# Optimization experiments

Measured on AMD Instinct MI355X. Metric: run time of the kernel, lower is better.

The kernel has to match this reference:

```python
import jax, jax.numpy as jnp
import numpy as np

NEG_SLOPE = 0.01
EPS = 1e-5


def leaky_relu(x):
    return jnp.where(x >= 0, x, NEG_SLOPE * x)


def graph_conv(x, W, src, dst, edge_weight, num_nodes):
    # DGL GraphConv, norm='both', bias=False: D_out^{-1/2} A_w D_in^{-1/2} X W
    ones = jnp.ones_like(edge_weight)
    deg_out = jnp.maximum(jax.ops.segment_sum(ones, src, num_segments=num_nodes), 1.0)
    deg_in = jnp.maximum(jax.ops.segment_sum(ones, dst, num_segments=num_nodes), 1.0)
    h = x @ W
    h = h * jax.lax.rsqrt(deg_out)[:, None]
    agg = jax.ops.segment_sum(h[src] * edge_weight[:, None], dst, num_segments=num_nodes)
    return agg * jax.lax.rsqrt(deg_in)[:, None]


def graph_norm(x, alpha, gamma, beta, batch_size):
    # GraphNorm: per-graph, per-channel mean/var; graphs are equal-sized -> reshape
    n = x.shape[0] // batch_size
    xg = x.reshape(batch_size, n, x.shape[1])
    mean = xg.mean(axis=1, keepdims=True)
    sub = xg - alpha * mean
    var = (sub * sub).mean(axis=1, keepdims=True)
    out = gamma * sub * jax.lax.rsqrt(var + EPS) + beta
    return out.reshape(x.shape)


def instance_norm(x):
    # InstanceNorm1d (affine=False) on 2D input: per-row normalization over features
    mean = x.mean(axis=-1, keepdims=True)
    var = ((x - mean) ** 2).mean(axis=-1, keepdims=True)
    return (x - mean) * jax.lax.rsqrt(var + EPS)


def setup_inputs() -> dict:
    key = jax.random.key(0)
    ks = jax.random.split(key, 9)
    B, n = 4096, 64                      # graphs, nodes per graph (equal-sized)
    N = B * n                            # 262144 nodes
    E = 8 * N                            # avg degree 8
    in_feats, conv_dim, out_conv = 64, 128, 96
    in_mlp = out_conv * n                # 6144 = in_feats_mlp
    hid = 2048
    out_feats = 256

    def kaiming(k, fin, fout):
        bound = float(np.sqrt(6.0 / ((1 + NEG_SLOPE ** 2) * fin)))
        return jax.random.uniform(k, (fin, fout), jnp.float32, -bound, bound)

    def xavier(k, fin, fout):
        bound = float(np.sqrt(6.0 / (fin + fout)))
        return jax.random.uniform(k, (fin, fout), jnp.float32, -bound, bound)

    return {
        "x": jax.random.normal(ks[0], (N, in_feats), jnp.float32),
        "edge_weight": jax.random.uniform(ks[1], (E,), jnp.float32),
        "src": jax.random.randint(ks[2], (E,), 0, N, jnp.int32),
        "dst": jax.random.randint(ks[3], (E,), 0, N, jnp.int32),
        "W1": kaiming(ks[4], in_feats, conv_dim),
        "W2": kaiming(ks[5], conv_dim, out_conv),
        "gn1_alpha": jnp.ones((conv_dim,), jnp.float32),
        "gn1_gamma": jnp.ones((conv_dim,), jnp.float32),
        "gn1_beta": jnp.zeros((conv_dim,), jnp.float32),
        "gn2_alpha": jnp.ones((out_conv,), jnp.float32),
        "gn2_gamma": jnp.ones((out_conv,), jnp.float32),
        "gn2_beta": jnp.zeros((out_conv,), jnp.float32),
        "Win": xavier(ks[6], in_mlp, hid),
        "Whid": xavier(ks[7], hid, hid // 4),
        "Wcls": xavier(ks[8], hid // 4, out_feats),
        "batch_size": B,
    }


def reference(x, edge_weight, src, dst, W1, W2, gn1_alpha, gn1_gamma, gn1_beta,
              gn2_alpha, gn2_gamma, gn2_beta, Win, Whid, Wcls, batch_size):
    N = x.shape[0]
    h = graph_conv(x, W1, src, dst, edge_weight, N)
    h = leaky_relu(h)
    h = graph_norm(h, gn1_alpha, gn1_gamma, gn1_beta, batch_size)
    h = graph_conv(h, W2, src, dst, edge_weight, N)
    h = leaky_relu(h)
    h = graph_norm(h, gn2_alpha, gn2_gamma, gn2_beta, batch_size)
    # unbatch: each equal-size graph flattened to one row [B, n*out_conv]
    h = h.reshape(batch_size, -1)
    h = instance_norm(leaky_relu(h @ Win))   # dropout is identity (p=0 / eval)
    h = instance_norm(leaky_relu(h @ Whid))
    return h @ Wcls
```

## Files before the change

kernel.cpp:

```cpp
#include <hip/hip_runtime.h>
#include <hip/hip_bf16.h>

#define NN 262144
#define EE 2097152
#define BB 4096
constexpr int INMLP = 6144;
constexpr int HID = 2048;
constexpr int HID4 = 512;
constexpr int OUTF = 256;
constexpr int NSL = 64;
constexpr int ESL = EE / NSL;
constexpr int RNODES = 32768;

typedef short s16x8 __attribute__((ext_vector_type(8)));
typedef short s16x4 __attribute__((ext_vector_type(4)));
typedef float f32x4 __attribute__((ext_vector_type(4)));

__device__ __forceinline__ float lrelu(float v) { return v >= 0.f ? v : 0.01f * v; }
__device__ __forceinline__ float bf2f(short s) {
    unsigned int u = ((unsigned int)(unsigned short)s) << 16;
    return __builtin_bit_cast(float, u);
}
__device__ __forceinline__ short f2bf(float f) {
    unsigned int u = __builtin_bit_cast(unsigned int, f);
    u = (u + 0x7fff + ((u >> 16) & 1)) >> 16;
    return (short)u;
}
__device__ __forceinline__ void async16(const void* g, void* l) {
    __builtin_amdgcn_global_load_lds((__attribute__((address_space(1))) void*)g,
                                     (__attribute__((address_space(3))) void*)l, 16, 0, 0);
}

__global__ __launch_bounds__(256) void hist_count(const int* __restrict__ dst, const int* __restrict__ src,
                                                  unsigned* __restrict__ part_din, unsigned* __restrict__ part_dout,
                                                  unsigned short* __restrict__ rankpack16) {
    __shared__ unsigned hist[RNODES / 2];
    const int S = blockIdx.x & 63;
    const int R = (blockIdx.x >> 6) & 7;
    const int T = blockIdx.x >> 9;
    for (int i = threadIdx.x; i < RNODES / 2; i += 256) hist[i] = 0;
    __syncthreads();
    const int* idxarr = T ? src : dst;
    const int4* v4 = (const int4*)(idxarr + S * ESL);
#pragma unroll 4
    for (int i = 0; i < ESL / 4 / 256; i++) {
        const int q0 = i * 256 + threadIdx.x;
        int4 q = v4[q0];
        const int ebase = S * ESL + q0 * 4;
#pragma unroll
        for (int k = 0; k < 4; k++) {
            int idx = k == 0 ? q.x : k == 1 ? q.y : k == 2 ? q.z : q.w;
            if ((idx >> 15) == R) {
                int local = idx & (RNODES - 1);
                unsigned old = atomicAdd(&hist[local >> 1], 1u << ((local & 1) * 16));
                if (T == 0) {
                    unsigned rank = (old >> ((local & 1) * 16)) & 0xffffu;
                    rankpack16[ebase + k] = (unsigned short)((S << 10) | rank);
                }
            }
        }
    }
    __syncthreads();
    unsigned* dp = (T ? part_dout : part_din) + (size_t)S * (NN / 2) + R * (RNODES / 2);
    for (int i = threadIdx.x; i < RNODES / 2; i += 256) dp[i] = hist[i];
}

__global__ __launch_bounds__(256) void deg_reduce(const unsigned* __restrict__ part_din,
                                                  const unsigned* __restrict__ part_dout,
                                                  unsigned* __restrict__ repbase_w,
                                                  float* __restrict__ ro, float* __restrict__ ri,
                                                  int* __restrict__ din) {
    int i = blockIdx.x * 256 + threadIdx.x;
    unsigned runl = 0, runh = 0, dl = 0, dh = 0;
#pragma unroll 8
    for (int S = 0; S < NSL; S++) {
        repbase_w[(size_t)S * (NN / 2) + i] = (runl & 0xffffu) | (runh << 16);
        unsigned w = part_din[(size_t)S * (NN / 2) + i];
        runl += w & 0xffffu; runh += w >> 16;
        unsigned w2 = part_dout[(size_t)S * (NN / 2) + i];
        dl += w2 & 0xffffu; dh += w2 >> 16;
    }
    int n0 = 2 * i, n1 = 2 * i + 1;
    din[n0] = (int)runl; din[n1] = (int)runh;
    ro[n0] = rsqrtf((float)(dl < 1u ? 1u : dl));
    ro[n1] = rsqrtf((float)(dh < 1u ? 1u : dh));
    ri[n0] = rsqrtf((float)(runl < 1u ? 1u : runl));
    ri[n1] = rsqrtf((float)(runh < 1u ? 1u : runh));
}

__global__ __launch_bounds__(256) void scanA(const int* __restrict__ cnt, int* __restrict__ blks) {
    __shared__ int s[256];
    int t = threadIdx.x;
    int i0 = blockIdx.x * 1024 + t * 4;
    int ts = cnt[i0] + cnt[i0 + 1] + cnt[i0 + 2] + cnt[i0 + 3];
    s[t] = ts; __syncthreads();
    for (int d = 128; d > 0; d >>= 1) { if (t < d) s[t] += s[t + d]; __syncthreads(); }
    if (t == 0) blks[blockIdx.x] = s[0];
}

__global__ __launch_bounds__(256) void scanB(int* __restrict__ blks, int* __restrict__ offN) {
    __shared__ int s[256];
    int t = threadIdx.x;
    int v = blks[t]; s[t] = v; __syncthreads();
    for (int d = 1; d < 256; d <<= 1) {
        int x = (t >= d) ? s[t - d] : 0; __syncthreads();
        s[t] += x; __syncthreads();
    }
    blks[t] = s[t] - v;
    if (t == 255) *offN = s[255];
}

__global__ __launch_bounds__(256) void scanC(const int* __restrict__ cnt, const int* __restrict__ blkoff,
                                             int* __restrict__ off) {
    __shared__ int s[256];
    int t = threadIdx.x;
    int i0 = blockIdx.x * 1024 + t * 4;
    int v0 = cnt[i0], v1 = cnt[i0 + 1], v2 = cnt[i0 + 2], v3 = cnt[i0 + 3];
    int ts = v0 + v1 + v2 + v3;
    s[t] = ts; __syncthreads();
    for (int d = 1; d < 256; d <<= 1) {
        int x = (t >= d) ? s[t - d] : 0; __syncthreads();
        s[t] += x; __syncthreads();
    }
    int base = blkoff[blockIdx.x] + (s[t] - ts);
    off[i0] = base; off[i0 + 1] = base + v0; off[i0 + 2] = base + v0 + v1; off[i0 + 3] = base + v0 + v1 + v2;
}

__global__ __launch_bounds__(256) void fill_csr(const int* __restrict__ src, const int* __restrict__ dst,
                                                const float* __restrict__ ew, const float* __restrict__ ro,
                                                const int* __restrict__ off,
                                                const unsigned short* __restrict__ repbase16,
                                                const unsigned short* __restrict__ rankpack16,
                                                int2* __restrict__ edg) {
    int e = blockIdx.x * 256 + threadIdx.x;
    int d = dst[e];
    int s = src[e];
    unsigned pk = rankpack16[e];
    int S = pk >> 10, rank = pk & 1023;
    int p = off[d] + (int)repbase16[(size_t)S * NN + d] + rank;
    edg[p] = make_int2(s, __builtin_bit_cast(int, ew[e] * ro[s]));
}

__global__ __launch_bounds__(256) void cvt_x(const float* __restrict__ X, short* __restrict__ Xb) {
    int i = (blockIdx.x * 256 + threadIdx.x) * 4;
    float4 v = *(const float4*)(X + i);
    s16x4 o = { f2bf(v.x), f2bf(v.y), f2bf(v.z), f2bf(v.w) };
    *(s16x4*)(Xb + i) = o;
}

__global__ __launch_bounds__(256) void gather64(const short* __restrict__ Xb, const int* __restrict__ offs,
                                                const int2* __restrict__ edg, short* __restrict__ Out) {
    const int lane = threadIdx.x & 63;
    const int e = lane >> 3, c = lane & 7;
    int node = blockIdx.x * 4 + (threadIdx.x >> 6);
    node = __builtin_amdgcn_readfirstlane(node);
    const int s0 = offs[node], s1 = offs[node + 1];
    float acc[8] = {};
    for (int j0 = s0; j0 < s1; j0 += 8) {
        int j = j0 + e;
        bool ok = j < s1;
        int2 pe = edg[ok ? j : s0];
        int s = pe.x;
        float w = ok ? __builtin_bit_cast(float, pe.y) : 0.f;
        s16x8 v = *(const s16x8*)&Xb[(size_t)s * 64 + c * 8];
#pragma unroll
        for (int k = 0; k < 8; k++) acc[k] = fmaf(w, bf2f(v[k]), acc[k]);
    }
#pragma unroll
    for (int off = 8; off <= 32; off <<= 1)
#pragma unroll
        for (int k = 0; k < 8; k++) acc[k] += __shfl_xor(acc[k], off);
    if (e == 0) {
        s16x8 o;
#pragma unroll
        for (int k = 0; k < 8; k++) o[k] = f2bf(acc[k]);
        *(s16x8*)&Out[(size_t)node * 64 + c * 8] = o;
    }
}

__global__ __launch_bounds__(256) void gather96(const short* __restrict__ H, const int* __restrict__ offs,
                                                const int2* __restrict__ edg, short* __restrict__ Out) {
    const int lane = threadIdx.x & 63;
    const int e = lane >> 4, c = lane & 15;
    int node = blockIdx.x * 4 + (threadIdx.x >> 6);
    node = __builtin_amdgcn_readfirstlane(node);
    const int s0 = offs[node], s1 = offs[node + 1];
    float acc[6] = {};
    for (int j0 = s0; j0 < s1; j0 += 4) {
        int j = j0 + e;
        bool ok = j < s1;
        int2 pe = edg[ok ? j : s0];
        int s = pe.x;
        float w = ok ? __builtin_bit_cast(float, pe.y) : 0.f;
        const unsigned int* hp = (const unsigned int*)(H + (size_t)s * 96 + c * 6);
        unsigned int u0 = hp[0], u1 = hp[1], u2 = hp[2];
        acc[0] = fmaf(w, bf2f((short)(u0 & 0xffff)), acc[0]);
        acc[1] = fmaf(w, bf2f((short)(u0 >> 16)), acc[1]);
        acc[2] = fmaf(w, bf2f((short)(u1 & 0xffff)), acc[2]);
        acc[3] = fmaf(w, bf2f((short)(u1 >> 16)), acc[3]);
        acc[4] = fmaf(w, bf2f((short)(u2 & 0xffff)), acc[4]);
        acc[5] = fmaf(w, bf2f((short)(u2 >> 16)), acc[5]);
    }
#pragma unroll
    for (int off = 16; off <= 32; off <<= 1)
#pragma unroll
        for (int k = 0; k < 6; k++) acc[k] += __shfl_xor(acc[k], off);
    if (e == 0) {
        unsigned int* op = (unsigned int*)(Out + (size_t)node * 96 + c * 6);
        op[0] = (unsigned short)f2bf(acc[0]) | ((unsigned)(unsigned short)f2bf(acc[1]) << 16);
        op[1] = (unsigned short)f2bf(acc[2]) | ((unsigned)(unsigned short)f2bf(acc[3]) << 16);
        op[2] = (unsigned short)f2bf(acc[4]) | ((unsigned)(unsigned short)f2bf(acc[5]) << 16);
    }
}

template <int C>
__global__ __launch_bounds__(256) void graphnorm_k(short* __restrict__ Ag, const float* __restrict__ ri,
                                                   const float* __restrict__ alpha, const float* __restrict__ gamma,
                                                   const float* __restrict__ beta) {
    __shared__ float sm[64 * C];
    __shared__ float sscale[C], sshift[C];
    const int g = blockIdx.x;
    const size_t base = (size_t)g * 64 * C;
    for (int idx = threadIdx.x; idx < 64 * C; idx += 256) {
        int i = idx / C;
        float v = bf2f(Ag[base + idx]) * ri[g * 64 + i];
        sm[idx] = lrelu(v);
    }
    __syncthreads();
    if (threadIdx.x < C) {
        int c = threadIdx.x;
        float s1 = 0.f, s2 = 0.f;
#pragma unroll 4
        for (int i = 0; i < 64; i++) { float v = sm[i * C + c]; s1 += v; s2 += v * v; }
        float m = s1 * (1.f / 64.f);
        float a = alpha[c];
        float var = s2 * (1.f / 64.f) - m * m * a * (2.f - a);
        float sc = gamma[c] * rsqrtf(var + 1e-5f);
        sscale[c] = sc;
        sshift[c] = beta[c] - sc * a * m;
    }
    __syncthreads();
    for (int idx = threadIdx.x; idx < 64 * C; idx += 256) {
        int c = idx % C;
        Ag[base + idx] = f2bf(sscale[c] * sm[idx] + sshift[c]);
    }
}

__global__ __launch_bounds__(256) void conv1_gn(const short* __restrict__ A, const short* __restrict__ BT,
                                                const float* __restrict__ ri,
                                                const float* __restrict__ alpha, const float* __restrict__ gamma,
                                                const float* __restrict__ beta, short* __restrict__ Outp) {
    __shared__ short As[128][72];
    __shared__ short Bs[128][72];
    __shared__ float sscale[2][128], sshift[2][128];
    const int t = threadIdx.x;
    const int bm = blockIdx.x * 128;
    const int wave = t >> 6, lane = t & 63;
    const int wm = (wave & 1) * 64, wn = (wave >> 1) * 64;
    const int g = wave & 1;
    const int m16 = lane & 15, quad = lane >> 4;
#pragma unroll
    for (int i = 0; i < 4; i++) {
        int idx = t + 256 * i;
        int rr = idx >> 3, kk = (idx & 7) * 8;
        *(s16x8*)&As[rr][kk] = *(const s16x8*)&A[(size_t)(bm + rr) * 64 + kk];
        *(s16x8*)&Bs[rr][kk] = *(const s16x8*)&BT[(size_t)rr * 64 + kk];
    }
    __syncthreads();
    f32x4 acc[4][4] = {};
#pragma unroll
    for (int kc = 0; kc < 2; kc++) {
        s16x8 af[4], bfr[4];
#pragma unroll
        for (int mt = 0; mt < 4; mt++) af[mt] = *(const s16x8*)&As[wm + mt * 16 + m16][kc * 32 + quad * 8];
#pragma unroll
        for (int nt = 0; nt < 4; nt++) bfr[nt] = *(const s16x8*)&Bs[wn + nt * 16 + m16][kc * 32 + quad * 8];
#pragma unroll
        for (int mt = 0; mt < 4; mt++)
#pragma unroll
            for (int nt = 0; nt < 4; nt++)
                acc[mt][nt] = __builtin_amdgcn_mfma_f32_16x16x32_bf16(af[mt], bfr[nt], acc[mt][nt], 0, 0, 0);
    }
#pragma unroll
    for (int mt = 0; mt < 4; mt++)
#pragma unroll
        for (int r4 = 0; r4 < 4; r4++) {
            float rv = ri[bm + wm + mt * 16 + quad * 4 + r4];
#pragma unroll
            for (int nt = 0; nt < 4; nt++)
                acc[mt][nt][r4] = lrelu(acc[mt][nt][r4] * rv);
        }
#pragma unroll
    for (int nt = 0; nt < 4; nt++) {
        float s1 = 0.f, s2 = 0.f;
#pragma unroll
        for (int mt = 0; mt < 4; mt++)
#pragma unroll
            for (int r4 = 0; r4 < 4; r4++) { float v = acc[mt][nt][r4]; s1 += v; s2 += v * v; }
        s1 += __shfl_xor(s1, 16); s1 += __shfl_xor(s1, 32);
        s2 += __shfl_xor(s2, 16); s2 += __shfl_xor(s2, 32);
        if (quad == 0) {
            int ch = wn + nt * 16 + m16;
            float m = s1 * (1.f / 64.f);
            float a = alpha[ch];
            float var = s2 * (1.f / 64.f) - m * m * a * (2.f - a);
            float sc = gamma[ch] * rsqrtf(var + 1e-5f);
            sscale[g][ch] = sc;
            sshift[g][ch] = beta[ch] - sc * a * m;
        }
    }
    __syncthreads();
#pragma unroll
    for (int nt = 0; nt < 4; nt++) {
        int ch = wn + nt * 16 + m16;
        float sc = sscale[g][ch], sh = sshift[g][ch];
#pragma unroll
        for (int mt = 0; mt < 4; mt++)
#pragma unroll
            for (int r4 = 0; r4 < 4; r4++) {
                int row = bm + wm + mt * 16 + quad * 4 + r4;
                Outp[(size_t)row * 128 + ch] = f2bf(sc * acc[mt][nt][r4] + sh);
            }
    }
}

__global__ __launch_bounds__(256) void conv2_mfma(const short* __restrict__ A, const short* __restrict__ BT,
                                                  short* __restrict__ H) {
    __shared__ short As[128][136];
    __shared__ short Bs[96][136];
    const int t = threadIdx.x;
    const int bm = blockIdx.x * 128;
    const int wave = t >> 6, lane = t & 63;
    const int wm = (wave & 1) * 64, wn = (wave >> 1) * 48;
    const int m16 = lane & 15, quad = lane >> 4;
#pragma unroll
    for (int i = 0; i < 8; i++) {
        int idx = t + 256 * i;
        int rr = idx >> 4, kk = (idx & 15) * 8;
        *(s16x8*)&As[rr][kk] = *(const s16x8*)&A[(size_t)(bm + rr) * 128 + kk];
    }
#pragma unroll
    for (int i = 0; i < 6; i++) {
        int idx = t + 256 * i;
        int nr = idx >> 4, kk = (idx & 15) * 8;
        *(s16x8*)&Bs[nr][kk] = *(const s16x8*)&BT[(size_t)nr * 128 + kk];
    }
    __syncthreads();
    f32x4 acc[4][3] = {};
#pragma unroll
    for (int kc = 0; kc < 4; kc++) {
        s16x8 af[4], bfr[3];
#pragma unroll
        for (int mt = 0; mt < 4; mt++) af[mt] = *(const s16x8*)&As[wm + mt * 16 + m16][kc * 32 + quad * 8];
#pragma unroll
        for (int nt = 0; nt < 3; nt++) bfr[nt] = *(const s16x8*)&Bs[wn + nt * 16 + m16][kc * 32 + quad * 8];
#pragma unroll
        for (int mt = 0; mt < 4; mt++)
#pragma unroll
            for (int nt = 0; nt < 3; nt++)
                acc[mt][nt] = __builtin_amdgcn_mfma_f32_16x16x32_bf16(af[mt], bfr[nt], acc[mt][nt], 0, 0, 0);
    }
#pragma unroll
    for (int mt = 0; mt < 4; mt++)
#pragma unroll
        for (int r4 = 0; r4 < 4; r4++) {
            int row = bm + wm + mt * 16 + quad * 4 + r4;
#pragma unroll
            for (int nt = 0; nt < 3; nt++)
                H[(size_t)row * 96 + wn + nt * 16 + m16] = f2bf(acc[mt][nt][r4]);
        }
}

__global__ __launch_bounds__(256) void transp_cvt(const float* __restrict__ W, short* __restrict__ WT,
                                                  int R, int Cc) {
    __shared__ short tile[32][33];
    const int bc = blockIdx.x * 32;
    const int br = blockIdx.y * 32;
    const int tx = threadIdx.x & 31, ty = threadIdx.x >> 5;
#pragma unroll
    for (int i = 0; i < 32; i += 8)
        tile[ty + i][tx] = f2bf(W[(size_t)(br + ty + i) * Cc + bc + tx]);
    __syncthreads();
#pragma unroll
    for (int i = 0; i < 32; i += 8)
        WT[(size_t)(bc + ty + i) * R + br + tx] = tile[tx][ty + i];
}

__global__ __launch_bounds__(256) void mlp1_mfma(const short* __restrict__ A, const short* __restrict__ BT,
                                                 short* __restrict__ Cp) {
    constexpr int K = INMLP, Nn = HID;
    __shared__ short As[128 * 64];
    __shared__ short Bs[128 * 64];
    const int t = threadIdx.x;
    const int bm = blockIdx.x * 128, bn = blockIdx.y * 128;
    const int kbase = blockIdx.z * (K / 2);
    const int wave = t >> 6, lane = t & 63;
    const int wm = (wave & 1) * 64, wn = (wave >> 1) * 64;
    const int m16 = lane & 15, quad = lane >> 4;
    const int lrow = lane >> 3, lcol = lane & 7;
    const int scol = lcol ^ (lrow & 7);
    const int xkey = m16 & 7;
    f32x4 acc[4][4] = {};
    for (int k0 = kbase; k0 < kbase + K / 2; k0 += 64) {
#pragma unroll
        for (int j = 0; j < 4; j++) {
            const int rbase = 32 * wave + 8 * j;
            async16(&A[(size_t)(bm + rbase + lrow) * K + k0 + scol * 8], &As[rbase * 64]);
            async16(&BT[(size_t)(bn + rbase + lrow) * K + k0 + scol * 8], &Bs[rbase * 64]);
        }
        __syncthreads();
#pragma unroll
        for (int kc = 0; kc < 2; kc++) {
            s16x8 af[4], bfr[4];
#pragma unroll
            for (int mt = 0; mt < 4; mt++)
                af[mt] = *(const s16x8*)&As[(wm + mt * 16 + m16) * 64 + (((kc * 4 + quad) ^ xkey)) * 8];
#pragma unroll
            for (int nt = 0; nt < 4; nt++)
                bfr[nt] = *(const s16x8*)&Bs[(wn + nt * 16 + m16) * 64 + (((kc * 4 + quad) ^ xkey)) * 8];
#pragma unroll
            for (int mt = 0; mt < 4; mt++)
#pragma unroll
                for (int nt = 0; nt < 4; nt++)
                    acc[mt][nt] = __builtin_amdgcn_mfma_f32_16x16x32_bf16(af[mt], bfr[nt], acc[mt][nt], 0, 0, 0);
        }
        __syncthreads();
    }
    short* C = Cp + (size_t)blockIdx.z * BB * HID;
#pragma unroll
    for (int mt = 0; mt < 4; mt++)
#pragma unroll
        for (int nt = 0; nt < 4; nt++)
#pragma unroll
            for (int r4 = 0; r4 < 4; r4++) {
                int row = bm + wm + mt * 16 + quad * 4 + r4;
                int col = bn + wn + nt * 16 + m16;
                C[(size_t)row * Nn + col] = f2bf(acc[mt][nt][r4]);
            }
}

__global__ __launch_bounds__(256) void rownorm_hid(short* __restrict__ D0, const short* __restrict__ D1) {
    const size_t base = (size_t)blockIdx.x * HID;
    float v[8];
    float s1 = 0.f, s2 = 0.f;
    const int c0 = threadIdx.x * 8;
    {
        s16x8 a = *(const s16x8*)&D0[base + c0];
        s16x8 b = *(const s16x8*)&D1[base + c0];
#pragma unroll
        for (int k = 0; k < 8; k++) {
            float x = lrelu(bf2f(a[k]) + bf2f(b[k]));
            v[k] = x; s1 += x; s2 += x * x;
        }
    }
#pragma unroll
    for (int o = 32; o > 0; o >>= 1) { s1 += __shfl_down(s1, o); s2 += __shfl_down(s2, o); }
    __shared__ float w1[4], w2[4];
    if ((threadIdx.x & 63) == 0) { w1[threadIdx.x >> 6] = s1; w2[threadIdx.x >> 6] = s2; }
    __syncthreads();
    s1 = w1[0] + w1[1] + w1[2] + w1[3];
    s2 = w2[0] + w2[1] + w2[2] + w2[3];
    float m = s1 * (1.f / HID);
    float inv = rsqrtf(s2 * (1.f / HID) - m * m + 1e-5f);
    s16x8 o;
#pragma unroll
    for (int k = 0; k < 8; k++) o[k] = f2bf((v[k] - m) * inv);
    *(s16x8*)&D0[base + c0] = o;
}

template <bool ABF16, bool LEAKY>
__global__ __launch_bounds__(256) void mfma_gemm(const float* __restrict__ Af, const short* __restrict__ Ab,
                                                 const short* __restrict__ BT,
                                                 float* __restrict__ C, int M, int Nn, int K) {
    __shared__ short As[64][40];
    __shared__ short Bs[64][40];
    const int t = threadIdx.x;
    const int bm = blockIdx.x * 64, bn = blockIdx.y * 64;
    const int wave = t >> 6, lane = t & 63;
    const int wm = (wave & 1) * 32, wn = (wave >> 1) * 32;
    const int m16 = lane & 15, quad = lane >> 4;
    const int rr = t >> 2, kk = (t & 3) * 8;
    f32x4 acc[2][2] = {};
    for (int k0 = 0; k0 < K; k0 += 32) {
        if (ABF16) {
            *(s16x8*)&As[rr][kk] = *(const s16x8*)&Ab[(size_t)(bm + rr) * K + k0 + kk];
        } else {
            const float* ap = &Af[(size_t)(bm + rr) * K + k0 + kk];
            float4 v0 = *(const float4*)ap;
            float4 v1 = *(const float4*)(ap + 4);
            s16x8 a8;
            a8[0] = f2bf(v0.x); a8[1] = f2bf(v0.y); a8[2] = f2bf(v0.z); a8[3] = f2bf(v0.w);
            a8[4] = f2bf(v1.x); a8[5] = f2bf(v1.y); a8[6] = f2bf(v1.z); a8[7] = f2bf(v1.w);
            *(s16x8*)&As[rr][kk] = a8;
        }
        *(s16x8*)&Bs[rr][kk] = *(const s16x8*)&BT[(size_t)(bn + rr) * K + k0 + kk];
        __syncthreads();
        s16x8 af[2], bfr[2];
#pragma unroll
        for (int mt = 0; mt < 2; mt++) af[mt] = *(const s16x8*)&As[wm + mt * 16 + m16][quad * 8];
#pragma unroll
        for (int nt = 0; nt < 2; nt++) bfr[nt] = *(const s16x8*)&Bs[wn + nt * 16 + m16][quad * 8];
#pragma unroll
        for (int mt = 0; mt < 2; mt++)
#pragma unroll
            for (int nt = 0; nt < 2; nt++)
                acc[mt][nt] = __builtin_amdgcn_mfma_f32_16x16x32_bf16(af[mt], bfr[nt], acc[mt][nt], 0, 0, 0);
        __syncthreads();
    }
#pragma unroll
    for (int mt = 0; mt < 2; mt++)
#pragma unroll
        for (int nt = 0; nt < 2; nt++)
#pragma unroll
            for (int r4 = 0; r4 < 4; r4++) {
                int row = bm + wm + mt * 16 + quad * 4 + r4;
                int col = bn + wn + nt * 16 + m16;
                float v = acc[mt][nt][r4];
                if (LEAKY) v = lrelu(v);
                C[(size_t)row * Nn + col] = v;
            }
}

template <int NC>
__global__ __launch_bounds__(256) void rownorm(float* __restrict__ Y) {
    float* p = Y + (size_t)blockIdx.x * NC;
    float s1 = 0.f, s2 = 0.f;
    for (int c = threadIdx.x; c < NC; c += 256) { float v = p[c]; s1 += v; s2 += v * v; }
#pragma unroll
    for (int o = 32; o > 0; o >>= 1) { s1 += __shfl_down(s1, o); s2 += __shfl_down(s2, o); }
    __shared__ float w1[4], w2[4];
    if ((threadIdx.x & 63) == 0) { w1[threadIdx.x >> 6] = s1; w2[threadIdx.x >> 6] = s2; }
    __syncthreads();
    s1 = w1[0] + w1[1] + w1[2] + w1[3];
    s2 = w2[0] + w2[1] + w2[2] + w2[3];
    float m = s1 * (1.f / NC);
    float inv = rsqrtf(s2 * (1.f / NC) - m * m + 1e-5f);
    for (int c = threadIdx.x; c < NC; c += 256) p[c] = (p[c] - m) * inv;
}

extern "C" void kernel_launch(void* const* d_in, const int* in_sizes, int n_in,
                              void* d_out, int out_size, void* d_ws, size_t ws_size,
                              hipStream_t stream) {
    const float* x    = (const float*)d_in[0];
    const float* ew   = (const float*)d_in[1];
    const int*   src  = (const int*)d_in[2];
    const int*   dst  = (const int*)d_in[3];
    const float* W1   = (const float*)d_in[4];
    const float* W2   = (const float*)d_in[5];
    const float* a1   = (const float*)d_in[6];
    const float* g1   = (const float*)d_in[7];
    const float* b1   = (const float*)d_in[8];
    const float* a2   = (const float*)d_in[9];
    const float* g2   = (const float*)d_in[10];
    const float* b2   = (const float*)d_in[11];
    const float* Win  = (const float*)d_in[12];
    const float* Whid = (const float*)d_in[13];
    const float* Wcls = (const float*)d_in[14];
    float* out = (float*)d_out;

    float* ro   = (float*)d_ws;
    float* ri   = ro + NN;
    int*   din  = (int*)(ri + NN);
    int*   offs = din + NN;
    int*   blks = offs + NN + 4;
    short* w1t  = (short*)(blks + 256);
    short* w2t  = w1t + 128 * 64;
    int2*  edg  = (int2*)(((size_t)(w2t + 96 * 128) + 15) & ~(size_t)15);
    short* Abf  = (short*)(edg + EE);
    short* Bbf  = Abf + (size_t)NN * 128;
    short* xbf  = Abf;
    short* aggx = Abf + (size_t)NN * 64;
    unsigned*       part_din   = (unsigned*)Abf;
    unsigned*       part_dout  = part_din + (size_t)NSL * (NN / 2);
    unsigned*       repbase_w  = (unsigned*)Bbf;
    unsigned short* rankpack16 = (unsigned short*)(repbase_w + (size_t)NSL * (NN / 2));
    short* WinT = Abf;
    short* D0   = (short*)((char*)Abf + 25165824);
    short* D1   = D0 + (size_t)BB * HID;
    float* Y2   = (float*)edg;
    short* WhidT = Bbf;
    short* WclsT = WhidT + (size_t)HID4 * HID;

    hist_count<<<2 * 8 * NSL, 256, 0, stream>>>(dst, src, part_din, part_dout, rankpack16);
    deg_reduce<<<NN / 512, 256, 0, stream>>>(part_din, part_dout, repbase_w, ro, ri, din);

    scanA<<<NN / 1024, 256, 0, stream>>>(din, blks);
    scanB<<<1, 256, 0, stream>>>(blks, offs + NN);
    scanC<<<NN / 1024, 256, 0, stream>>>(din, blks, offs);
    fill_csr<<<EE / 256, 256, 0, stream>>>(src, dst, ew, ro, offs,
                                           (const unsigned short*)repbase_w, rankpack16, edg);

    cvt_x<<<NN * 64 / 1024, 256, 0, stream>>>(x, xbf);
    transp_cvt<<<dim3(128 / 32, 64 / 32), 256, 0, stream>>>(W1, w1t, 64, 128);
    gather64<<<NN / 4, 256, 0, stream>>>(xbf, offs, edg, aggx);
    conv1_gn<<<NN / 128, 256, 0, stream>>>(aggx, w1t, ri, a1, g1, b1, Bbf);

    transp_cvt<<<dim3(96 / 32, 128 / 32), 256, 0, stream>>>(W2, w2t, 128, 96);
    conv2_mfma<<<NN / 128, 256, 0, stream>>>(Bbf, w2t, Abf);
    gather96<<<NN / 4, 256, 0, stream>>>(Abf, offs, edg, Bbf);
    graphnorm_k<96><<<BB, 256, 0, stream>>>(Bbf, ri, a2, g2, b2);

    transp_cvt<<<dim3(HID / 32, INMLP / 32), 256, 0, stream>>>(Win, WinT, INMLP, HID);
    mlp1_mfma<<<dim3(BB / 128, HID / 128, 2), 256, 0, stream>>>(Bbf, WinT, D0);
    transp_cvt<<<dim3(HID4 / 32, HID / 32), 256, 0, stream>>>(Whid, WhidT, HID, HID4);
    transp_cvt<<<dim3(OUTF / 32, HID4 / 32), 256, 0, stream>>>(Wcls, WclsT, HID4, OUTF);
    rownorm_hid<<<BB, 256, 0, stream>>>(D0, D1);
    mfma_gemm<true, true><<<dim3(BB / 64, HID4 / 64), 256, 0, stream>>>(nullptr, D0, WhidT, Y2, BB, HID4, HID);
    rownorm<HID4><<<BB, 256, 0, stream>>>(Y2);
    mfma_gemm<false, false><<<dim3(BB / 64, OUTF / 64), 256, 0, stream>>>(Y2, nullptr, WclsT, out, BB, OUTF, HID4);
}
```

Measured before the change: 831.4 us.

## Rewrite MLP1 GEMM as 256x256-tile, 8-wave, double-buffered ping-pong pipeline

Replaces the 128x128 tile MLP1 GEMM (4 waves, single LDS buffer, full syncthreads per k-step) with a 256x256 tile kernel using 8 waves, double-buffered LDS and interleaved async global loads between MFMA clusters. It adds explicit barriers, waitcnt control, sched barriers and setprio to overlap memory with compute, plus a swizzled block-to-tile mapping for L2 locality. Larger tiles raise arithmetic intensity, at the cost of 128KB LDS per block and fewer blocks (256) across the CUs, so occupancy and load balance are the risks.

Measured after the change: 944.7 us. +13.6%, slower.

```diff
diff --git a/kernel.cpp b/kernel.cpp
--- a/kernel.cpp
+++ b/kernel.cpp
@@ -386,57 +386,109 @@
         WT[(size_t)(bc + ty + i) * R + br + tx] = tile[tx][ty + i];
 }
 
-__global__ __launch_bounds__(256) void mlp1_mfma(const short* __restrict__ A, const short* __restrict__ BT,
-                                                 short* __restrict__ Cp) {
-    constexpr int K = INMLP, Nn = HID;
-    __shared__ short As[128 * 64];
-    __shared__ short Bs[128 * 64];
+#define MBAR() __builtin_amdgcn_s_barrier()
+#define LGKM0() asm volatile("s_waitcnt lgkmcnt(0)" ::: "memory")
+#define SB0() __builtin_amdgcn_sched_barrier(0)
+
+__global__ __launch_bounds__(512, 2) void mlp1_mfma8(const short* __restrict__ A, const short* __restrict__ BT,
+                                                     short* __restrict__ Cp) {
+    constexpr int K = INMLP;
+    __shared__ short As[2][256 * 64];
+    __shared__ short Bs[2][256 * 64];
     const int t = threadIdx.x;
-    const int bm = blockIdx.x * 128, bn = blockIdx.y * 128;
-    const int kbase = blockIdx.z * (K / 2);
-    const int wave = t >> 6, lane = t & 63;
-    const int wm = (wave & 1) * 64, wn = (wave >> 1) * 64;
-    const int m16 = lane & 15, quad = lane >> 4;
+    const int wid = t >> 6, lane = t & 63;
     const int lrow = lane >> 3, lcol = lane & 7;
     const int scol = lcol ^ (lrow & 7);
-    const int xkey = m16 & 7;
-    f32x4 acc[4][4] = {};
-    for (int k0 = kbase; k0 < kbase + K / 2; k0 += 64) {
-#pragma unroll
-        for (int j = 0; j < 4; j++) {
-            const int rbase = 32 * wave + 8 * j;
-            async16(&A[(size_t)(bm + rbase + lrow) * K + k0 + scol * 8], &As[rbase * 64]);
-            async16(&BT[(size_t)(bn + rbase + lrow) * K + k0 + scol * 8], &Bs[rbase * 64]);
-        }
-        __syncthreads();
-#pragma unroll
-        for (int kc = 0; kc < 2; kc++) {
-            s16x8 af[4], bfr[4];
-#pragma unroll
-            for (int mt = 0; mt < 4; mt++)
-                af[mt] = *(const s16x8*)&As[(wm + mt * 16 + m16) * 64 + (((kc * 4 + quad) ^ xkey)) * 8];
-#pragma unroll
-            for (int nt = 0; nt < 4; nt++)
-                bfr[nt] = *(const s16x8*)&Bs[(wn + nt * 16 + m16) * 64 + (((kc * 4 + quad) ^ xkey)) * 8];
-#pragma unroll
-            for (int mt = 0; mt < 4; mt++)
-#pragma unroll
-                for (int nt = 0; nt < 4; nt++)
-                    acc[mt][nt] = __builtin_amdgcn_mfma_f32_16x16x32_bf16(af[mt], bfr[nt], acc[mt][nt], 0, 0, 0);
-        }
-        __syncthreads();
-    }
-    short* C = Cp + (size_t)blockIdx.z * BB * HID;
-#pragma unroll
-    for (int mt = 0; mt < 4; mt++)
+    const int m16 = lane & 15, quad = lane >> 4, xkey = m16 & 7;
+    const int wm = wid & 1, wn = wid >> 1;
+    const int sw = (blockIdx.x & 7) * 32 + (blockIdx.x >> 3);
+    const int bm = sw & 15, bn = (sw >> 4) & 7, z = sw >> 7;
+    const short* gA = A + (size_t)(bm * 256 + wid * 32 + lrow) * K + (size_t)z * (K / 2) + scol * 8;
+    const short* gB = BT + (size_t)(bn * 256 + wid * 16 + lrow) * K + (size_t)z * (K / 2) + scol * 8;
+
+    s16x8 a0[8], a1[8], b0[4], b1[4];
+    f32x4 acc[8][4] = {};
+
+#define STAGE_A(s, ko) \
+    { _Pragma("unroll") for (int j = 0; j < 4; j++) \
+        async16(gA + (size_t)(j * 8) * K + (ko), &As[s][(wid * 32 + j * 8) * 64]); }
+#define STAGE_B(s, ko, h) \
+    { _Pragma("unroll") for (int j = 0; j < 2; j++) \
+        async16(gB + (size_t)((h) * 128 + j * 8) * K + (ko), &Bs[s][((h) * 128 + wid * 16 + j * 8) * 64]); }
+#define LD_A(s, kc, d) \
+    { _Pragma("unroll") for (int mt = 0; mt < 8; mt++) \
+        d[mt] = *(const s16x8*)&As[s][(wm * 128 + mt * 16 + m16) * 64 + (((kc) * 4 + quad) ^ xkey) * 8]; }
+#define LD_B(s, kc, d) \
+    { _Pragma("unroll") for (int nt = 0; nt < 4; nt++) \
+        d[nt] = *(const s16x8*)&Bs[s][(wn * 64 + nt * 16 + m16) * 64 + (((kc) * 4 + quad) ^ xkey) * 8]; }
+#define MM2(a, b, nlo) \
+    { _Pragma("unroll") for (int mt = 0; mt < 8; mt++) { \
+        acc[mt][(nlo)] = __builtin_amdgcn_mfma_f32_16x16x32_bf16(a[mt], b[(nlo)], acc[mt][(nlo)], 0, 0, 0); \
+        acc[mt][(nlo) + 1] = __builtin_amdgcn_mfma_f32_16x16x32_bf16(a[mt], b[(nlo) + 1], acc[mt][(nlo) + 1], 0, 0, 0); } }
+
+    STAGE_A(0, 0); STAGE_B(0, 0, 0); STAGE_B(0, 0, 1);
+    STAGE_B(1, 64, 0); STAGE_B(1, 64, 1); STAGE_A(1, 64);
+    asm volatile("s_waitcnt vmcnt(8)" ::: "memory");
+    MBAR();
+
+    int kof = 0;
+#pragma unroll 1
+    for (int i = 0; i < 24; i++, kof += 128) {
+        const bool st = (i < 23);
+        LD_A(0, 0, a0); LD_B(0, 0, b0);
+        MBAR(); LGKM0(); SB0();
+        __builtin_amdgcn_s_setprio(1); MM2(a0, b0, 0); __builtin_amdgcn_s_setprio(0);
+        MBAR();
+        LD_A(0, 1, a1); LD_B(0, 1, b1);
+        MBAR(); LGKM0(); SB0();
+        __builtin_amdgcn_s_setprio(1); MM2(a0, b0, 2); __builtin_amdgcn_s_setprio(0);
+        MBAR();
+        if (st) STAGE_A(0, kof + 128);
+        MBAR(); LGKM0(); SB0();
+        __builtin_amdgcn_s_setprio(1); MM2(a1, b1, 0); __builtin_amdgcn_s_setprio(0);
+        if (st) { asm volatile("s_waitcnt vmcnt(4)" ::: "memory"); }
+        else    { asm volatile("s_waitcnt vmcnt(0)" ::: "memory"); }
+        MBAR();
+        LD_A(1, 0, a0); LD_B(1, 0, b0);
+        if (st) STAGE_B(0, kof + 128, 0);
+        MBAR(); LGKM0(); SB0();
+        __builtin_amdgcn_s_setprio(1); MM2(a1, b1, 2); __builtin_amdgcn_s_setprio(0);
+        MBAR();
+        LD_A(1, 1, a1); LD_B(1, 1, b1);
+        if (st) STAGE_B(0, kof + 128, 1);
+        MBAR(); LGKM0(); SB0();
+        __builtin_amdgcn_s_setprio(1); MM2(a0, b0, 0); __builtin_amdgcn_s_setprio(0);
+        MBAR();
+        if (st) STAGE_B(1, kof + 192, 0);
+        MBAR(); LGKM0(); SB0();
+        __builtin_amdgcn_s_setprio(1); MM2(a0, b0, 2); __builtin_amdgcn_s_setprio(0);
+        MBAR();
+        if (st) STAGE_B(1, kof + 192, 1);
+        MBAR(); LGKM0(); SB0();
+        __builtin_amdgcn_s_setprio(1); MM2(a1, b1, 0); __builtin_amdgcn_s_setprio(0);
+        MBAR();
+        if (st) STAGE_A(1, kof + 192);
+        MBAR(); LGKM0(); SB0();
+        __builtin_amdgcn_s_setprio(1); MM2(a1, b1, 2); __builtin_amdgcn_s_setprio(0);
+        if (st) { asm volatile("s_waitcnt vmcnt(8)" ::: "memory"); }
+        MBAR();
+    }
+
+    short* C = Cp + (size_t)z * BB * HID;
+    const int r0 = bm * 256 + wm * 128 + quad * 4;
+    const int c0 = bn * 256 + wn * 64 + m16;
+#pragma unroll
+    for (int mt = 0; mt < 8; mt++)
 #pragma unroll
         for (int nt = 0; nt < 4; nt++)
 #pragma unroll
-            for (int r4 = 0; r4 < 4; r4++) {
-                int row = bm + wm + mt * 16 + quad * 4 + r4;
-                int col = bn + wn + nt * 16 + m16;
-                C[(size_t)row * Nn + col] = f2bf(acc[mt][nt][r4]);
-            }
+            for (int r4 = 0; r4 < 4; r4++)
+                C[(size_t)(r0 + mt * 16 + r4) * HID + c0 + nt * 16] = f2bf(acc[mt][nt][r4]);
+#undef STAGE_A
+#undef STAGE_B
+#undef LD_A
+#undef LD_B
+#undef MM2
 }
 
 __global__ __launch_bounds__(256) void rownorm_hid(short* __restrict__ D0, const short* __restrict__ D1) {
@@ -601,7 +653,7 @@
     graphnorm_k<96><<<BB, 256, 0, stream>>>(Bbf, ri, a2, g2, b2);
 
     transp_cvt<<<dim3(HID / 32, INMLP / 32), 256, 0, stream>>>(Win, WinT, INMLP, HID);
-    mlp1_mfma<<<dim3(BB / 128, HID / 128, 2), 256, 0, stream>>>(Bbf, WinT, D0);
+    mlp1_mfma8<<<256, 512, 0, stream>>>(Bbf, WinT, D0);
     transp_cvt<<<dim3(HID4 / 32, HID / 32), 256, 0, stream>>>(Whid, WhidT, HID, HID4);
     transp_cvt<<<dim3(OUTF / 32, HID4 / 32), 256, 0, stream>>>(Wcls, WclsT, HID4, OUTF);
     rownorm_hid<<<BB, 256, 0, stream>>>(D0, D1);
```
